# Kernel optimization log

Measured on AMD Instinct MI355X. Metric: run time of the kernel, lower is better.

Reference implementation:

```python
import jax, jax.numpy as jnp
import numpy as np

N_NODES = 100000


def gcn_conv(x, edge_index, W, b):
    # PyG GCNConv: add self-loops, symmetric normalization, then scatter-add.
    n = x.shape[0]
    loops = jnp.arange(n, dtype=edge_index.dtype)
    src = jnp.concatenate([edge_index[0], loops])
    dst = jnp.concatenate([edge_index[1], loops])
    h = x @ W  # [N, F_out] -- transform before propagate (small GEMM)
    ones = jnp.ones(src.shape[0], dtype=x.dtype)
    deg = jax.ops.segment_sum(ones, dst, num_segments=n)  # in-degree incl. self-loop
    dinv = jnp.where(deg > 0, jax.lax.rsqrt(deg), 0.0)
    norm = dinv[src] * dinv[dst]  # [E+N]
    msg = h[src] * norm[:, None]  # gather + scale, [E+N, F_out]
    out = jax.ops.segment_sum(msg, dst, num_segments=n)  # scatter-add
    return out + b


def setup_inputs() -> dict:
    key = jax.random.key(0)
    k1, k2, k3, k4 = jax.random.split(key, 4)
    d = 128
    x = jax.random.normal(k1, (N_NODES, d), dtype=jnp.float32)
    edge_index = jax.random.randint(k2, (2, 1600000), 0, N_NODES, dtype=jnp.int64)
    scale = 1.0 / np.sqrt(d)
    W1 = jax.random.normal(k3, (d, d), dtype=jnp.float32) * scale
    b1 = jnp.zeros((d,), dtype=jnp.float32)
    W2 = jax.random.normal(k4, (d, d), dtype=jnp.float32) * scale
    b2 = jnp.zeros((d,), dtype=jnp.float32)
    return {"x": x, "edge_index": edge_index, "W1": W1, "b1": b1, "W2": W2, "b2": b2}


def reference(x, edge_index, W1, b1, W2, b2):
    # Layer 1: GCNConv -> relu -> dropout(eval: identity)
    h = jax.nn.relu(gcn_conv(x, edge_index, W1, b1))
    # Layer 2
    h = jax.nn.relu(gcn_conv(h, edge_index, W2, b2))
    return h
```

## Files before the change

### kernel.cpp

```cpp
#include <hip/hip_runtime.h>


#define NFEAT 128
#define BSH 7
#define MAXNB 1024
#define BCAP 4096
#define HP 72
#define YP 132

typedef __attribute__((ext_vector_type(8))) short s8v;
typedef __attribute__((ext_vector_type(4))) float f4v;
typedef __attribute__((ext_vector_type(2))) float f2v;
typedef __attribute__((ext_vector_type(4))) uint u4v;

__device__ inline ushort f2bf(float f) {
    union { float f; uint u; } x; x.f = f;
    uint u = x.u;
    return (ushort)((u + 0x7fffu + ((u >> 16) & 1u)) >> 16);
}
__device__ inline f2v unpk(uint u) {
    union { uint u; float f; } lo, hi;
    lo.u = u << 16;
    hi.u = u & 0xffff0000u;
    return (f2v){lo.f, hi.f};
}
__device__ inline void upfma2(uint4 v, float g, f2v* a) {
    a[0] += g * unpk(v.x);
    a[1] += g * unpk(v.y);
    a[2] += g * unpk(v.z);
    a[3] += g * unpk(v.w);
}

__device__ inline void node_gather(const uint4* __restrict__ hs4,
                                   const int* __restrict__ row_ptr,
                                   const int* __restrict__ col,
                                   const float* __restrict__ dinv,
                                   int node, int sub, f2v* a) {
    uint4 vself = hs4[(size_t)node * 16 + sub];
    float dself = dinv[node];
    int s = row_ptr[node], e = row_ptr[node + 1];
    int nb = (e - s) >> 2;
    int k = s;
    if (nb > 0) {
        int c0 = col[k], c1 = col[k + 1], c2 = col[k + 2], c3 = col[k + 3];
        uint4 v0 = hs4[(size_t)c0 * 16 + sub];
        uint4 v1 = hs4[(size_t)c1 * 16 + sub];
        uint4 v2 = hs4[(size_t)c2 * 16 + sub];
        uint4 v3 = hs4[(size_t)c3 * 16 + sub];
        float g0 = dinv[c0], g1 = dinv[c1], g2 = dinv[c2], g3 = dinv[c3];
        int d0 = col[k + 4], d1 = col[k + 5], d2 = col[k + 6], d3 = col[k + 7];
        k += 8;
        upfma2(vself, dself, a);
        for (int it = 1; it < nb; ++it, k += 4) {
            uint4 w0 = hs4[(size_t)d0 * 16 + sub];
            uint4 w1 = hs4[(size_t)d1 * 16 + sub];
            uint4 w2 = hs4[(size_t)d2 * 16 + sub];
            uint4 w3 = hs4[(size_t)d3 * 16 + sub];
            float h0 = dinv[d0], h1 = dinv[d1], h2 = dinv[d2], h3 = dinv[d3];
            int t0 = col[k], t1 = col[k + 1], t2 = col[k + 2], t3 = col[k + 3];
            upfma2(v0, g0, a); upfma2(v1, g1, a); upfma2(v2, g2, a); upfma2(v3, g3, a);
            v0 = w0; v1 = w1; v2 = w2; v3 = w3;
            g0 = h0; g1 = h1; g2 = h2; g3 = h3;
            d0 = t0; d1 = t1; d2 = t2; d3 = t3;
        }
        upfma2(v0, g0, a); upfma2(v1, g1, a); upfma2(v2, g2, a); upfma2(v3, g3, a);
        k = s + nb * 4;
    } else {
        upfma2(vself, dself, a);
    }
    for (; k < e; ++k) {
        int c = col[k];
        upfma2(hs4[(size_t)c * 16 + sub], dinv[c], a);
    }
}

__device__ inline void stage_w_half(ushort* Bs, const float* __restrict__ W, int h, int t) {
#pragma unroll
    for (int i = 0; i < 8; i++) {
        int idx = t + i * 256;
        int k4 = idx >> 7;
        int n = idx & 127;
        ushort o[4];
#pragma unroll
        for (int j = 0; j < 4; j++) o[j] = f2bf(W[(h * 64 + k4 * 4 + j) * NFEAT + n]);
        uint2 pk;
        __builtin_memcpy(&pk, o, 8);
        *(uint2*)&Bs[n * HP + k4 * 4] = pk;
    }
}

template <bool ABF16>
__device__ inline void gemm_body(ushort* Bs, int bid, const void* __restrict__ Ap,
                                 const float* __restrict__ W,
                                 ushort* __restrict__ hs, int M) {
    int t = threadIdx.x;
    int w = t >> 6, l = t & 63;
    int q = l >> 4, ln = l & 15;
    int row0 = (bid * 4 + w) * 16;

    int arow = row0 + ln;
    if (arow >= M) arow = M - 1;
    s8v afr[4];
    if (ABF16) {
        const ushort* A = (const ushort*)Ap + (size_t)arow * NFEAT + q * 8;
#pragma unroll
        for (int g = 0; g < 4; g++) afr[g] = *(const s8v*)(A + g * 32);
    } else {
        const float* A = (const float*)Ap + (size_t)arow * NFEAT + q * 8;
#pragma unroll
        for (int g = 0; g < 4; g++) {
            float4 f0 = *(const float4*)(A + g * 32);
            float4 f1 = *(const float4*)(A + g * 32 + 4);
            ushort o[8] = {f2bf(f0.x), f2bf(f0.y), f2bf(f0.z), f2bf(f0.w),
                           f2bf(f1.x), f2bf(f1.y), f2bf(f1.z), f2bf(f1.w)};
            __builtin_memcpy(&afr[g], o, 16);
        }
    }

    f4v acc[8];
#pragma unroll
    for (int nt = 0; nt < 8; nt++) acc[nt] = (f4v){0.f, 0.f, 0.f, 0.f};

#pragma unroll
    for (int h = 0; h < 2; h++) {
        if (h) __syncthreads();
        stage_w_half(Bs, W, h, t);
        __syncthreads();
#pragma unroll
        for (int nt = 0; nt < 8; nt++) {
            const ushort* Bp = Bs + (nt * 16 + ln) * HP + q * 8;
#pragma unroll
            for (int ks = 0; ks < 2; ks++) {
                s8v bfr = *(const s8v*)(Bp + ks * 32);
                acc[nt] = __builtin_amdgcn_mfma_f32_16x16x32_bf16(afr[h * 2 + ks], bfr, acc[nt], 0, 0, 0);
            }
        }
    }

#pragma unroll
    for (int r = 0; r < 4; r++) {
        int row = row0 + q * 4 + r;
        if (row < M) {
            ushort* hp = hs + (size_t)row * NFEAT + ln;
#pragma unroll
            for (int nt = 0; nt < 8; nt++) hp[nt * 16] = f2bf(acc[nt][r]);
        }
    }
}

__global__ __launch_bounds__(256) void k_fused1(const int* __restrict__ src,
                                                const int* __restrict__ dst,
                                                int* __restrict__ gcnt,
                                                uint* __restrict__ ebuf,
                                                int E, int NB, int CH, int chBlk,
                                                const float* __restrict__ x,
                                                const float* __restrict__ W1,
                                                ushort* __restrict__ hs, int M) {
    __shared__ __align__(16) ushort smem[128 * HP];
    int bid = blockIdx.x;
    int sid = bid / 3, r = bid % 3;
    if (r == 0 && sid < chBlk) {
        int* h = (int*)smem;
        int t = threadIdx.x;
        for (int i = t; i < NB; i += 256) h[i] = 0;
        __syncthreads();
        int e0 = sid * CH;
        int e1 = min(e0 + CH, E);
        for (int e = e0 + t; e < e1; e += 256) atomicAdd(&h[dst[e] >> BSH], 1);
        __syncthreads();
        for (int i = t; i < NB; i += 256) {
            int c = h[i];
            h[i] = c ? (i * BCAP + atomicAdd(&gcnt[i], c)) : 0;
        }
        __syncthreads();
        for (int e = e0 + t; e < e1; e += 256) {
            int d = dst[e];
            int b = d >> BSH;
            int p = atomicAdd(&h[b], 1);
            if (p < (b + 1) * BCAP)
                ebuf[p] = ((uint)src[e] << BSH) | (uint)(d & ((1 << BSH) - 1));
        }
    } else {
        int scats_before = min(sid + (r ? 1 : 0), chBlk);
        gemm_body<false>(smem, bid - scats_before, x, W1, hs, M);
    }
}

__global__ __launch_bounds__(256) void k_fill2(const uint* __restrict__ ebuf,
                                               const int* __restrict__ gcnt,
                                               int* __restrict__ row_ptr,
                                               float* __restrict__ dinv,
                                               int* __restrict__ col,
                                               int N, int E, int NB) {
    __shared__ int cnt[128];
    __shared__ int pre[128];
    __shared__ int sred[256];
    __shared__ int colL[BCAP];
    int b = blockIdx.x;
    int t = threadIdx.x;
    int part = 0;
    for (int j = t; j < b; j += 256) part += gcnt[j];
    sred[t] = part;
    __syncthreads();
    for (int off = 128; off >= 1; off >>= 1) {
        if (t < off) sred[t] += sred[t + off];
        __syncthreads();
    }
    int gb = sred[0];
    int m = min(gcnt[b], BCAP);
    if (t < 128) cnt[t] = 0;
    __syncthreads();
    const uint* eb = ebuf + (size_t)b * BCAP;
    for (int i = t; i < m; i += 256) atomicAdd(&cnt[eb[i] & 127], 1);
    __syncthreads();
    if (t < 128) pre[t] = cnt[t];
    __syncthreads();
    for (int off = 1; off < 128; off <<= 1) {
        int add = (t >= off && t < 128) ? pre[t - off] : 0;
        __syncthreads();
        if (t < 128) pre[t] += add;
        __syncthreads();
    }
    if (t < 128) {
        pre[t] -= cnt[t];
        int node = (b << BSH) + t;
        if (node < N) {
            row_ptr[node] = gb + pre[t];
            dinv[node] = rsqrtf((float)(cnt[t] + 1));
        }
    }
    __syncthreads();
    for (int i = t; i < m; i += 256) {
        uint p = eb[i];
        int pos = atomicAdd(&pre[p & 127], 1);
        colL[pos] = (int)(p >> BSH);
    }
    __syncthreads();
    for (int i = t; i < m; i += 256) col[gb + i] = colL[i];
    if (b == NB - 1 && t == 0) row_ptr[N] = E;
}

__global__ __launch_bounds__(256) void k_aggG(const uint4* __restrict__ hs4,
                                              const int* __restrict__ row_ptr,
                                              const int* __restrict__ col,
                                              const float* __restrict__ dinv,
                                              const float* __restrict__ bias,
                                              const float* __restrict__ W2,
                                              ushort* __restrict__ hs2, int N) {
    __shared__ __align__(16) ushort yT[64 * YP];
    __shared__ __align__(16) ushort Bs[128 * HP];
    int t = threadIdx.x;
    int grp = t >> 4, sub = t & 15;
    int base = blockIdx.x * 64;

    const float4* b4 = (const float4*)bias;
    float4 bb0 = b4[sub * 2], bb1 = b4[sub * 2 + 1];

    for (int i = 0; i < 4; i++) {
        int myn = grp + i * 16;
        int node = base + myn;
        uint4 pk = make_uint4(0, 0, 0, 0);
        if (node < N) {
            f2v a[4];
#pragma unroll
            for (int j = 0; j < 4; j++) a[j] = (f2v){0.f, 0.f};
            node_gather(hs4, row_ptr, col, dinv, node, sub, a);
            float di = dinv[node];
            ushort o[8];
            o[0] = f2bf(fmaxf(fmaf(di, a[0].x, bb0.x), 0.f));
            o[1] = f2bf(fmaxf(fmaf(di, a[0].y, bb0.y), 0.f));
            o[2] = f2bf(fmaxf(fmaf(di, a[1].x, bb0.z), 0.f));
            o[3] = f2bf(fmaxf(fmaf(di, a[1].y, bb0.w), 0.f));
            o[4] = f2bf(fmaxf(fmaf(di, a[2].x, bb1.x), 0.f));
            o[5] = f2bf(fmaxf(fmaf(di, a[2].y, bb1.y), 0.f));
            o[6] = f2bf(fmaxf(fmaf(di, a[3].x, bb1.z), 0.f));
            o[7] = f2bf(fmaxf(fmaf(di, a[3].y, bb1.w), 0.f));
            __builtin_memcpy(&pk, o, 16);
        }
        *(uint4*)&yT[myn * YP + sub * 8] = pk;
    }
    __syncthreads();

    int w = t >> 6, l = t & 63;
    int q = l >> 4, ln = l & 15;
    f4v acc[8];
#pragma unroll
    for (int nt = 0; nt < 8; nt++) acc[nt] = (f4v){0.f, 0.f, 0.f, 0.f};
#pragma unroll
    for (int h = 0; h < 2; h++) {
        if (h) __syncthreads();
        stage_w_half(Bs, W2, h, t);
        __syncthreads();
        s8v a2[2];
        a2[0] = *(const s8v*)&yT[(w * 16 + ln) * YP + (h * 2 + 0) * 32 + q * 8];
        a2[1] = *(const s8v*)&yT[(w * 16 + ln) * YP + (h * 2 + 1) * 32 + q * 8];
#pragma unroll
        for (int nt = 0; nt < 8; nt++) {
            const ushort* Bp = Bs + (nt * 16 + ln) * HP + q * 8;
#pragma unroll
            for (int ks = 0; ks < 2; ks++) {
                s8v bfr = *(const s8v*)(Bp + ks * 32);
                acc[nt] = __builtin_amdgcn_mfma_f32_16x16x32_bf16(a2[ks], bfr, acc[nt], 0, 0, 0);
            }
        }
    }
#pragma unroll
    for (int rr = 0; rr < 4; rr++) {
        int node = base + w * 16 + q * 4 + rr;
        if (node < N) {
            ushort* hp = hs2 + (size_t)node * NFEAT + ln;
#pragma unroll
            for (int nt = 0; nt < 8; nt++) hp[nt * 16] = f2bf(acc[nt][rr]);
        }
    }
}

template <bool OUT_BF16>
__global__ __launch_bounds__(256) void k_aggregate(const uint4* __restrict__ hs4,
                                                   const int* __restrict__ row_ptr,
                                                   const int* __restrict__ col,
                                                   const float* __restrict__ dinv,
                                                   const float* __restrict__ bias,
                                                   void* __restrict__ outp, int N) {
    int node = blockIdx.x * 16 + (threadIdx.x >> 4);
    if (node >= N) return;
    int sub = threadIdx.x & 15;

    f2v a[4];
#pragma unroll
    for (int j = 0; j < 4; j++) a[j] = (f2v){0.f, 0.f};
    node_gather(hs4, row_ptr, col, dinv, node, sub, a);

    float di = dinv[node];
    const float4* b4 = (const float4*)bias;
    float4 b0 = b4[sub * 2], b1 = b4[sub * 2 + 1];
    float r[8];
    r[0] = fmaxf(fmaf(di, a[0].x, b0.x), 0.f);
    r[1] = fmaxf(fmaf(di, a[0].y, b0.y), 0.f);
    r[2] = fmaxf(fmaf(di, a[1].x, b0.z), 0.f);
    r[3] = fmaxf(fmaf(di, a[1].y, b0.w), 0.f);
    r[4] = fmaxf(fmaf(di, a[2].x, b1.x), 0.f);
    r[5] = fmaxf(fmaf(di, a[2].y, b1.y), 0.f);
    r[6] = fmaxf(fmaf(di, a[3].x, b1.z), 0.f);
    r[7] = fmaxf(fmaf(di, a[3].y, b1.w), 0.f);
    if (OUT_BF16) {
        ushort o[8];
#pragma unroll
        for (int j = 0; j < 8; j++) o[j] = f2bf(r[j]);
        u4v pk;
        __builtin_memcpy(&pk, o, 16);
        __builtin_nontemporal_store(pk, (u4v*)outp + (size_t)node * 16 + sub);
    } else {
        float* orow = (float*)outp + (size_t)node * NFEAT + sub * 8;
        f4v r0 = {r[0], r[1], r[2], r[3]};
        f4v r1 = {r[4], r[5], r[6], r[7]};
        __builtin_nontemporal_store(r0, (f4v*)orow);
        __builtin_nontemporal_store(r1, (f4v*)(orow + 4));
    }
}

extern "C" void kernel_launch(void* const* d_in, const int* in_sizes, int n_in,
                              void* d_out, int out_size, void* d_ws, size_t ws_size,
                              hipStream_t stream) {
    const float* x = (const float*)d_in[0];
    const int* ei = (const int*)d_in[1];
    const float* W1 = (const float*)d_in[2];
    const float* b1 = (const float*)d_in[3];
    const float* W2 = (const float*)d_in[4];
    const float* b2 = (const float*)d_in[5];
    float* out = (float*)d_out;

    const int N = in_sizes[0] / NFEAT;
    const int E = in_sizes[1] / 2;
    const int* src = ei;
    const int* dst = ei + E;
    const int NB = (N + (1 << BSH) - 1) >> BSH;

    char* w = (char*)d_ws;
    size_t off = 0;
    auto alloc = [&](size_t bytes) -> void* {
        void* p = w + off;
        off = (off + bytes + 511) & ~(size_t)511;
        return p;
    };
    ushort* hs = (ushort*)alloc((size_t)N * NFEAT * 2);
    ushort* hs2 = (ushort*)alloc((size_t)N * NFEAT * 2);
    int* row_ptr = (int*)alloc((size_t)(N + 1) * 4);
    float* dinv = (float*)alloc((size_t)N * 4);
    int* col = (int*)alloc((size_t)(E + 64) * 4);
    uint* ebuf = (uint*)alloc((size_t)NB * BCAP * 4);
    int* gcnt = (int*)alloc((size_t)MAXNB * 4);
    (void)ws_size; (void)n_in; (void)out_size;

    const int CH = 2048;
    const int chBlk = (E + CH - 1) / CH;
    const int gemmBlk = (N + 63) / 64;
    const int aggBlk = (N + 15) / 16;

    hipMemsetAsync(gcnt, 0, (size_t)MAXNB * 4, stream);
    k_fused1<<<chBlk + gemmBlk, 256, 0, stream>>>(src, dst, gcnt, ebuf, E, NB, CH, chBlk,
                                                  x, W1, hs, N);
    k_fill2<<<NB, 256, 0, stream>>>(ebuf, gcnt, row_ptr, dinv, col, N, E, NB);

    k_aggG<<<gemmBlk, 256, 0, stream>>>((const uint4*)hs, row_ptr, col, dinv, b1, W2, hs2, N);
    k_aggregate<false><<<aggBlk, 256, 0, stream>>>((const uint4*)hs2, row_ptr, col, dinv, b2, out, N);
}
```

Baseline: 307.1 us.

## Sort edges locally in LDS before bucket scatter; fuse fill2 with layer-1 GEMM

Edge bucketing now runs as its own kernel. Each block of 4096 edges is counting-sorted by bucket in LDS, then written to the global bucket buffer so that writes within a bucket are contiguous, replacing scattered global writes. The CSR fill step is moved into a combined kernel that interleaves fill blocks with the layer-1 GEMM blocks, instead of fusing the GEMM with the scatter. The aggregation+GEMM kernel also preloads all A fragments into registers so it can reuse one LDS buffer for both tiles, which cuts its shared memory and may raise occupancy.

```diff
diff --git a/kernel.cpp b/kernel.cpp
--- a/kernel.cpp
+++ b/kernel.cpp
@@ -7,6 +7,7 @@
 #define BCAP 4096
 #define HP 72
 #define YP 132
+#define CH2 4096
 
 typedef __attribute__((ext_vector_type(8))) short s8v;
 typedef __attribute__((ext_vector_type(4))) float f4v;
@@ -89,6 +90,62 @@
     }
 }
 
+__global__ __launch_bounds__(256) void k_bsort(const int* __restrict__ src,
+                                               const int* __restrict__ dst,
+                                               int* __restrict__ gcnt,
+                                               uint* __restrict__ ebuf,
+                                               int E, int NB) {
+    __shared__ int cnt_[MAXNB];
+    __shared__ int loff[MAXNB];
+    __shared__ int gbase[MAXNB];
+    __shared__ int tsum[256];
+    __shared__ uint sv[CH2];
+    __shared__ ushort sb[CH2];
+
+    int t = threadIdx.x;
+    int e0 = blockIdx.x * CH2;
+    int m = min(CH2, E - e0);
+
+#pragma unroll
+    for (int i = t; i < MAXNB; i += 256) cnt_[i] = 0;
+    __syncthreads();
+    for (int e = e0 + t; e < e0 + m; e += 256) atomicAdd(&cnt_[dst[e] >> BSH], 1);
+    __syncthreads();
+    for (int b = t; b < NB; b += 256) {
+        int c = cnt_[b];
+        gbase[b] = c ? (b * BCAP + atomicAdd(&gcnt[b], c)) : 0;
+    }
+    int v0 = cnt_[t * 4], v1 = cnt_[t * 4 + 1], v2 = cnt_[t * 4 + 2], v3 = cnt_[t * 4 + 3];
+    int my = v0 + v1 + v2 + v3;
+    tsum[t] = my;
+    __syncthreads();
+    for (int off = 1; off < 256; off <<= 1) {
+        int add = (t >= off) ? tsum[t - off] : 0;
+        __syncthreads();
+        tsum[t] += add;
+        __syncthreads();
+    }
+    int run = tsum[t] - my;
+    loff[t * 4] = run; cnt_[t * 4] = run; run += v0;
+    loff[t * 4 + 1] = run; cnt_[t * 4 + 1] = run; run += v1;
+    loff[t * 4 + 2] = run; cnt_[t * 4 + 2] = run; run += v2;
+    loff[t * 4 + 3] = run; cnt_[t * 4 + 3] = run;
+    __syncthreads();
+    for (int e = e0 + t; e < e0 + m; e += 256) {
+        int d = dst[e];
+        int b = d >> BSH;
+        int p = atomicAdd(&cnt_[b], 1);
+        sv[p] = ((uint)src[e] << BSH) | (uint)(d & ((1 << BSH) - 1));
+        sb[p] = (ushort)b;
+    }
+    __syncthreads();
+    for (int i = t; i < m; i += 256) {
+        int b = sb[i];
+        int slot = gbase[b] + (i - loff[b]);
+        if (slot < (b + 1) * BCAP) ebuf[slot] = sv[i];
+    }
+}
+
 template <bool ABF16>
 __device__ inline void gemm_body(ushort* Bs, int bid, const void* __restrict__ Ap,
                                  const float* __restrict__ W,
@@ -148,55 +205,17 @@
     }
 }
 
-__global__ __launch_bounds__(256) void k_fused1(const int* __restrict__ src,
-                                                const int* __restrict__ dst,
-                                                int* __restrict__ gcnt,
-                                                uint* __restrict__ ebuf,
-                                                int E, int NB, int CH, int chBlk,
-                                                const float* __restrict__ x,
-                                                const float* __restrict__ W1,
-                                                ushort* __restrict__ hs, int M) {
-    __shared__ __align__(16) ushort smem[128 * HP];
-    int bid = blockIdx.x;
-    int sid = bid / 3, r = bid % 3;
-    if (r == 0 && sid < chBlk) {
-        int* h = (int*)smem;
-        int t = threadIdx.x;
-        for (int i = t; i < NB; i += 256) h[i] = 0;
-        __syncthreads();
-        int e0 = sid * CH;
-        int e1 = min(e0 + CH, E);
-        for (int e = e0 + t; e < e1; e += 256) atomicAdd(&h[dst[e] >> BSH], 1);
-        __syncthreads();
-        for (int i = t; i < NB; i += 256) {
-            int c = h[i];
-            h[i] = c ? (i * BCAP + atomicAdd(&gcnt[i], c)) : 0;
-        }
-        __syncthreads();
-        for (int e = e0 + t; e < e1; e += 256) {
-            int d = dst[e];
-            int b = d >> BSH;
-            int p = atomicAdd(&h[b], 1);
-            if (p < (b + 1) * BCAP)
-                ebuf[p] = ((uint)src[e] << BSH) | (uint)(d & ((1 << BSH) - 1));
-        }
-    } else {
-        int scats_before = min(sid + (r ? 1 : 0), chBlk);
-        gemm_body<false>(smem, bid - scats_before, x, W1, hs, M);
-    }
-}
-
-__global__ __launch_bounds__(256) void k_fill2(const uint* __restrict__ ebuf,
-                                               const int* __restrict__ gcnt,
-                                               int* __restrict__ row_ptr,
-                                               float* __restrict__ dinv,
-                                               int* __restrict__ col,
-                                               int N, int E, int NB) {
-    __shared__ int cnt[128];
-    __shared__ int pre[128];
-    __shared__ int sred[256];
-    __shared__ int colL[BCAP];
-    int b = blockIdx.x;
+__device__ inline void fill2_body(char* smem, int b,
+                                  const uint* __restrict__ ebuf,
+                                  const int* __restrict__ gcnt,
+                                  int* __restrict__ row_ptr,
+                                  float* __restrict__ dinv,
+                                  int* __restrict__ col,
+                                  int N, int E, int NB) {
+    int* cnt = (int*)smem;
+    int* pre = cnt + 128;
+    int* sred = pre + 128;
+    int* colL = sred + 256;
     int t = threadIdx.x;
     int part = 0;
     for (int j = t; j < b; j += 256) part += gcnt[j];
@@ -238,6 +257,27 @@
     __syncthreads();
     for (int i = t; i < m; i += 256) col[gb + i] = colL[i];
     if (b == NB - 1 && t == 0) row_ptr[N] = E;
+}
+
+__global__ __launch_bounds__(256) void k_fused2(const uint* __restrict__ ebuf,
+                                                const int* __restrict__ gcnt,
+                                                int* __restrict__ row_ptr,
+                                                float* __restrict__ dinv,
+                                                int* __restrict__ col,
+                                                int N, int E, int NB,
+                                                const float* __restrict__ x,
+                                                const float* __restrict__ W1,
+                                                ushort* __restrict__ hs) {
+    __shared__ __align__(16) char smem[18432];
+    int bid = blockIdx.x;
+    int r = bid % 3;
+    int fid = bid / 3;
+    if (r == 0 && fid < NB) {
+        fill2_body(smem, fid, ebuf, gcnt, row_ptr, dinv, col, N, E, NB);
+    } else {
+        int fills_before = min(fid + (r ? 1 : 0), NB);
+        gemm_body<false>((ushort*)smem, bid - fills_before, x, W1, hs, N);
+    }
 }
 
 __global__ __launch_bounds__(256) void k_aggG(const uint4* __restrict__ hs4,
@@ -247,8 +287,9 @@
                                               const float* __restrict__ bias,
                                               const float* __restrict__ W2,
                                               ushort* __restrict__ hs2, int N) {
-    __shared__ __align__(16) ushort yT[64 * YP];
-    __shared__ __align__(16) ushort Bs[128 * HP];
+    __shared__ __align__(16) ushort smem[128 * HP];
+    ushort* yT = smem;
+    ushort* Bs = smem;
     int t = threadIdx.x;
     int grp = t >> 4, sub = t & 15;
     int base = blockIdx.x * 64;
@@ -283,6 +324,12 @@
 
     int w = t >> 6, l = t & 63;
     int q = l >> 4, ln = l & 15;
+    s8v a2[4];
+#pragma unroll
+    for (int g = 0; g < 4; g++)
+        a2[g] = *(const s8v*)&yT[(w * 16 + ln) * YP + g * 32 + q * 8];
+    __syncthreads();
+
     f4v acc[8];
 #pragma unroll
     for (int nt = 0; nt < 8; nt++) acc[nt] = (f4v){0.f, 0.f, 0.f, 0.f};
@@ -291,16 +338,13 @@
         if (h) __syncthreads();
         stage_w_half(Bs, W2, h, t);
         __syncthreads();
-        s8v a2[2];
-        a2[0] = *(const s8v*)&yT[(w * 16 + ln) * YP + (h * 2 + 0) * 32 + q * 8];
-        a2[1] = *(const s8v*)&yT[(w * 16 + ln) * YP + (h * 2 + 1) * 32 + q * 8];
 #pragma unroll
         for (int nt = 0; nt < 8; nt++) {
             const ushort* Bp = Bs + (nt * 16 + ln) * HP + q * 8;
 #pragma unroll
             for (int ks = 0; ks < 2; ks++) {
                 s8v bfr = *(const s8v*)(Bp + ks * 32);
-                acc[nt] = __builtin_amdgcn_mfma_f32_16x16x32_bf16(a2[ks], bfr, acc[nt], 0, 0, 0);
+                acc[nt] = __builtin_amdgcn_mfma_f32_16x16x32_bf16(a2[h * 2 + ks], bfr, acc[nt], 0, 0, 0);
             }
         }
     }
@@ -392,16 +436,14 @@
     int* gcnt = (int*)alloc((size_t)MAXNB * 4);
     (void)ws_size; (void)n_in; (void)out_size;
 
-    const int CH = 2048;
-    const int chBlk = (E + CH - 1) / CH;
+    const int sortBlk = (E + CH2 - 1) / CH2;
     const int gemmBlk = (N + 63) / 64;
     const int aggBlk = (N + 15) / 16;
 
     hipMemsetAsync(gcnt, 0, (size_t)MAXNB * 4, stream);
-    k_fused1<<<chBlk + gemmBlk, 256, 0, stream>>>(src, dst, gcnt, ebuf, E, NB, CH, chBlk,
-                                                  x, W1, hs, N);
-    k_fill2<<<NB, 256, 0, stream>>>(ebuf, gcnt, row_ptr, dinv, col, N, E, NB);
-
+    k_bsort<<<sortBlk, 256, 0, stream>>>(src, dst, gcnt, ebuf, E, NB);
+    k_fused2<<<NB + gemmBlk, 256, 0, stream>>>(ebuf, gcnt, row_ptr, dinv, col, N, E, NB,
+                                               x, W1, hs);
     k_aggG<<<gemmBlk, 256, 0, stream>>>((const uint4*)hs, row_ptr, col, dinv, b1, W2, hs2, N);
     k_aggregate<false><<<aggBlk, 256, 0, stream>>>((const uint4*)hs2, row_ptr, col, dinv, b2, out, N);
 }
```

After: 301.3 us. About the same (-1.9%).
